# Performance work log

Hardware: AMD Instinct MI355X
Metric: run time of the kernel (lower is better)

The kernel has to match this reference:

```python
import jax, jax.numpy as jnp
import numpy as np

LEAKY_SLOPE = 0.2  # LeakyReLU(0.2) attention activation from the torch module
HEADS = 4
RATES = (10, 25)


def _prod(v):
    r = 1
    for x in v:
        r *= x
    return r


def gat_conv(x_self, x_neigh, W, a_s, a_n):
    """Single GAT aggregation layer (aggregate_method='concat').
    x_self:  [..., F_in]
    x_neigh: [..., E, F_in] (leading dims reshape-compatible with x_self)
    W: [F_in, H*D], a_s/a_n: [H, D]
    Returns [..., H*D].
    """
    H = HEADS
    D = W.shape[1] // H
    lead = x_self.shape[:-1]
    E = x_neigh.shape[-2]
    z_s = (x_self @ W).reshape(lead + (H, D))                  # [..., H, D]
    z_n = (x_neigh @ W).reshape(lead + (E, H, D))              # [..., E, H, D]
    e_s = jnp.einsum('...hd,hd->...h', z_s, a_s)               # [..., H]
    e_n = jnp.einsum('...ehd,hd->...eh', z_n, a_n)             # [..., E, H]
    logits = jax.nn.leaky_relu(e_s[..., None, :] + e_n, LEAKY_SLOPE)
    alpha = jax.nn.softmax(logits, axis=-2)                    # softmax over neighbors E
    out = jnp.einsum('...eh,...ehd->...hd', alpha, z_n)        # attention-weighted sum
    return out.reshape(lead + (H * D,))


def setup_inputs() -> dict:
    key = jax.random.key(0)
    ks = jax.random.split(key, 10)
    B, F, HID, OUT = 1024, 128, 512, 256
    s = 0.05
    return {
        'h0': jax.random.normal(ks[0], (B, F), jnp.float32),
        'h1': jax.random.normal(ks[1], (B, RATES[0], F), jnp.float32),
        'h2': jax.random.normal(ks[2], (B, RATES[0] * RATES[1], F), jnp.float32),
        'W0': jax.random.normal(ks[3], (F, HID), jnp.float32) * s,
        'a0_s': jax.random.normal(ks[4], (HEADS, HID // HEADS), jnp.float32) * s,
        'a0_n': jax.random.normal(ks[5], (HEADS, HID // HEADS), jnp.float32) * s,
        'W1': jax.random.normal(ks[6], (HID, HID), jnp.float32) * s,
        'a1_s': jax.random.normal(ks[7], (HEADS, HID // HEADS), jnp.float32) * s,
        'a1_n': jax.random.normal(ks[8], (HEADS, HID // HEADS), jnp.float32) * s,
        'W_fc': jax.random.normal(ks[9], (HID, OUT), jnp.float32) * s,
    }


def reference(h0, h1, h2, W0, a0_s, a0_n, W1, a1_s, a1_n, W_fc):
    B = h0.shape[0]
    hs = [h0, h1, h2]
    layers = [(W0, a0_s, a0_n), (W1, a1_s, a1_n)]
    depth = len(RATES)
    # hierarchical sweep: layer i is applied to levels 0..depth-i-1
    for i, (W, a_s, a_n) in enumerate(layers):
        for j in range(depth - i):
            x_self = hs[j]
            x_neigh = hs[j + 1].reshape(B, _prod(RATES[:j]), RATES[j], -1)
            hs[j] = gat_conv(x_self, x_neigh, W, a_s, a_n)
    return hs[0] @ W_fc  # final Linear (no bias, no activation)
```

## Files before the change

kernel.cpp:

```cpp
#include <hip/hip_runtime.h>

__global__ void __launch_bounds__(256) prep1(
    const float* __restrict__ W0, const float* __restrict__ a0s,
    const float* __restrict__ a0n,
    const float* __restrict__ W1, const float* __restrict__ a1s,
    const float* __restrict__ a1n, const float* __restrict__ Wfc,
    float* __restrict__ wa0s, float* __restrict__ wa0n,
    float* __restrict__ wa1s, float* __restrict__ wa1n,
    float* __restrict__ T) {
  int idx = blockIdx.x * 256 + threadIdx.x;
  if (idx < 5120) {
    const float* W; const float* a; float* dst; int i; int FIN;
    if (idx < 512)       { W = W0; a = a0s; dst = wa0s; i = idx;        FIN = 128; }
    else if (idx < 1024) { W = W0; a = a0n; dst = wa0n; i = idx - 512;  FIN = 128; }
    else if (idx < 3072) { W = W1; a = a1s; dst = wa1s; i = idx - 1024; FIN = 512; }
    else                 { W = W1; a = a1n; dst = wa1n; i = idx - 3072; FIN = 512; }
    int f = i >> 2, h = i & 3;
    const float* wrow = W + (size_t)f * 512 + h * 128;
    const float* arow = a + h * 128;
    float v = 0.f;
#pragma unroll 8
    for (int d = 0; d < 128; ++d) v = fmaf(wrow[d], arow[d], v);
    dst[h * FIN + f] = v;
    return;
  }
  int j = idx - 5120;
  if (j >= 4 * 512 * 256) return;
  int h = j >> 17;
  int k = (j >> 8) & 511;
  int o = j & 255;
  const float* w1row = W1 + (size_t)k * 512 + h * 128;
  const float* fcol = Wfc + (size_t)h * 128 * 256 + o;
  float v = 0.f;
#pragma unroll 8
  for (int m = 0; m < 128; ++m) v = fmaf(w1row[m], fcol[(size_t)m * 256], v);
  T[j] = v;
}

__global__ void __launch_bounds__(256) prep2(
    const float* __restrict__ W0, const float* __restrict__ wa1s,
    const float* __restrict__ wa1n, const float* __restrict__ T,
    float* __restrict__ va1s, float* __restrict__ va1n,
    float* __restrict__ Wfinal) {
  int idx = blockIdx.x * 256 + threadIdx.x;
  if (idx < 4096) {
    const float* wa = (idx < 2048) ? wa1s : wa1n;
    float* dst = (idx < 2048) ? va1s : va1n;
    int i = idx & 2047;
    int h = i >> 9, h0 = (i >> 7) & 3, f = i & 127;
    const float* w0row = W0 + (size_t)f * 512 + h0 * 128;
    const float* warow = wa + h * 512 + h0 * 128;
    float v = 0.f;
#pragma unroll 8
    for (int n = 0; n < 128; ++n) v = fmaf(w0row[n], warow[n], v);
    dst[i] = v;
    return;
  }
  int j = idx - 4096;
  if (j >= 4 * 512 * 256) return;
  int h = j >> 17;
  int kk = (j >> 8) & 511;
  int o = j & 255;
  int h0 = kk >> 7, f = kk & 127;
  const float* w0row = W0 + (size_t)f * 512 + h0 * 128;
  const float* tcol = T + (size_t)h * 512 * 256 + (size_t)(h0 * 128) * 256 + o;
  float v = 0.f;
#pragma unroll 8
  for (int n = 0; n < 128; ++n) v = fmaf(w0row[n], tcol[(size_t)n * 256], v);
  Wfinal[j] = v;
}

template <int FIN, int MR, int TPR>
__device__ __forceinline__ void gat_body(
    const float* __restrict__ xself, const float* __restrict__ xneigh,
    const float* __restrict__ waS, const float* __restrict__ waN,
    float* __restrict__ out, int E) {
  constexpr int RPP = 256 / TPR;
  constexpr int PSTR = TPR + 1;
  constexpr int G = TPR / 4;
  __shared__ float tile[MR * FIN];
  __shared__ float partial[MR * PSTR];
  __shared__ float logitS[MR * 4];
  __shared__ float alpha[(MR - 1) * 4];
  const int t = threadIdx.x;
  const int el = t / TPR;
  const int f0 = (t % TPR) * 4;
  float4 wn[4], ws[4];
#pragma unroll
  for (int h = 0; h < 4; ++h) {
    wn[h] = *reinterpret_cast<const float4*>(waN + h * FIN + f0);
    ws[h] = *reinterpret_cast<const float4*>(waS + h * FIN + f0);
  }
  const int rows = E + 1;
  for (int p = 0; p * RPP < rows; ++p) {
    int e = p * RPP + el;
    if (e < rows) {
      const float* src = (e < E) ? (xneigh + (size_t)e * FIN + f0) : (xself + f0);
      float4 x = *reinterpret_cast<const float4*>(src);
      *reinterpret_cast<float4*>(tile + e * FIN + f0) = x;
      float ph[4];
#pragma unroll
      for (int h = 0; h < 4; ++h) {
        float4 w = (e < E) ? wn[h] : ws[h];
        ph[h] = x.x * w.x + x.y * w.y + x.z * w.z + x.w * w.w;
      }
#pragma unroll
      for (int h = 0; h < 4; ++h) {
        ph[h] += __shfl_xor(ph[h], 1);
        ph[h] += __shfl_xor(ph[h], 2);
      }
      if ((t & 3) == 0) {
        int g = (t % TPR) >> 2;
        *reinterpret_cast<float4*>(partial + e * PSTR + g * 4) =
            make_float4(ph[0], ph[1], ph[2], ph[3]);
      }
    }
  }
  __syncthreads();
  if (t < rows * 4) {
    int e = t >> 2, h = t & 3;
    float v = 0.f;
#pragma unroll
    for (int g = 0; g < G; ++g) v += partial[e * PSTR + g * 4 + h];
    logitS[t] = v;
  }
  __syncthreads();
  if (t < 4) {
    const float es = logitS[E * 4 + t];
    float m = -1e30f;
    for (int e = 0; e < E; ++e) {
      float x = es + logitS[e * 4 + t];
      x = (x > 0.f) ? x : 0.2f * x;
      m = fmaxf(m, x);
    }
    float s = 0.f;
    for (int e = 0; e < E; ++e) {
      float x = es + logitS[e * 4 + t];
      x = (x > 0.f) ? x : 0.2f * x;
      float p = __expf(x - m);
      alpha[e * 4 + t] = p;
      s += p;
    }
    float inv = 1.f / s;
    for (int e = 0; e < E; ++e) alpha[e * 4 + t] *= inv;
  }
  __syncthreads();
  constexpr int C = FIN / 4;
  for (int o = t; o < 4 * C; o += 256) {
    int h = o / C, f = (o % C) * 4;
    float4 acc = make_float4(0.f, 0.f, 0.f, 0.f);
#pragma unroll 5
    for (int e = 0; e < E; ++e) {
      float a = alpha[e * 4 + h];
      float4 x = *reinterpret_cast<const float4*>(tile + e * FIN + f);
      acc.x = fmaf(a, x.x, acc.x);
      acc.y = fmaf(a, x.y, acc.y);
      acc.z = fmaf(a, x.z, acc.z);
      acc.w = fmaf(a, x.w, acc.w);
    }
    *reinterpret_cast<float4*>(out + h * FIN + f) = acc;
  }
}

__global__ void __launch_bounds__(256) gat_layer0(
    const float* __restrict__ h0, const float* __restrict__ h1,
    const float* __restrict__ h2, const float* __restrict__ waS,
    const float* __restrict__ waN, float* __restrict__ xagg) {
  const int b = blockIdx.x;
  const float* xself;
  const float* xneigh;
  int E;
  if (b < 1024) {
    E = 10;
    xself = h0 + (size_t)b * 128;
    xneigh = h1 + (size_t)b * 10 * 128;
  } else {
    int g = b - 1024;
    E = 25;
    xself = h1 + (size_t)g * 128;
    xneigh = h2 + (size_t)g * 25 * 128;
  }
  gat_body<128, 26, 32>(xself, xneigh, waS, waN, xagg + (size_t)b * 512, E);
}

__global__ void __launch_bounds__(256) gat_layer1(
    const float* __restrict__ xagg0, const float* __restrict__ xagg1,
    const float* __restrict__ vaS, const float* __restrict__ vaN,
    float* __restrict__ aggx) {
  const int b = blockIdx.x;
  gat_body<512, 11, 128>(xagg0 + (size_t)b * 512, xagg1 + (size_t)b * 10 * 512,
                         vaS, vaN, aggx + (size_t)b * 2048, 10);
}

__global__ void __launch_bounds__(256) gemm_ksplit(
    const float* __restrict__ A, int lda,
    const float* __restrict__ B, int ldb,
    float* __restrict__ Cpart, int ldc, int Kchunk) {
  __shared__ float As[16][68];
  __shared__ float Bs[16][132];
  const int m0 = blockIdx.x * 64;
  const int hb = blockIdx.y;
  const int ks = blockIdx.z;
  const int col0 = hb * 128;
  const float* Ab = A + (size_t)m0 * lda + (size_t)ks * Kchunk;
  const float* Bb = B + (size_t)ks * Kchunk * ldb + col0;
  float* Cb = Cpart + (size_t)ks * 1024 * 256;
  const int t = threadIdx.x;
  const int tn = t & 31, tm = t >> 5;
  const int lam = t >> 2, lak = (t & 3) * 4;
  const int lbk = t >> 4, lbn = (t & 15) * 8;
  float acc[8][4];
#pragma unroll
  for (int i = 0; i < 8; ++i)
#pragma unroll
    for (int j = 0; j < 4; ++j) acc[i][j] = 0.f;
  for (int k0 = 0; k0 < Kchunk; k0 += 16) {
    float4 av = *reinterpret_cast<const float4*>(Ab + (size_t)lam * lda + k0 + lak);
    As[lak + 0][lam] = av.x;
    As[lak + 1][lam] = av.y;
    As[lak + 2][lam] = av.z;
    As[lak + 3][lam] = av.w;
    const float* bp = Bb + (size_t)(k0 + lbk) * ldb + lbn;
    float4 b0 = *reinterpret_cast<const float4*>(bp);
    float4 b1 = *reinterpret_cast<const float4*>(bp + 4);
    float* bd = &Bs[lbk][lbn];
    bd[0] = b0.x; bd[1] = b0.y; bd[2] = b0.z; bd[3] = b0.w;
    bd[4] = b1.x; bd[5] = b1.y; bd[6] = b1.z; bd[7] = b1.w;
    __syncthreads();
#pragma unroll
    for (int kk = 0; kk < 16; ++kk) {
      float4 a0 = *reinterpret_cast<const float4*>(&As[kk][tm * 8]);
      float4 a1 = *reinterpret_cast<const float4*>(&As[kk][tm * 8 + 4]);
      float4 bv = *reinterpret_cast<const float4*>(&Bs[kk][tn * 4]);
      float a[8] = {a0.x, a0.y, a0.z, a0.w, a1.x, a1.y, a1.z, a1.w};
      float b[4] = {bv.x, bv.y, bv.z, bv.w};
#pragma unroll
      for (int i = 0; i < 8; ++i)
#pragma unroll
        for (int j = 0; j < 4; ++j) acc[i][j] = fmaf(a[i], b[j], acc[i][j]);
    }
    __syncthreads();
  }
#pragma unroll
  for (int i = 0; i < 8; ++i) {
    const int m = m0 + tm * 8 + i;
    float* cp = Cb + (size_t)m * ldc + col0 + tn * 4;
    *reinterpret_cast<float4*>(cp) =
        make_float4(acc[i][0], acc[i][1], acc[i][2], acc[i][3]);
  }
}

__global__ void __launch_bounds__(256) reduce8(
    const float* __restrict__ Cpart, float* __restrict__ out) {
  int i = blockIdx.x * 256 + threadIdx.x;
  const float4* p = reinterpret_cast<const float4*>(Cpart) + i;
  float4 s = p[0];
#pragma unroll
  for (int ks = 1; ks < 8; ++ks) {
    float4 v = p[(size_t)ks * 65536];
    s.x += v.x; s.y += v.y; s.z += v.z; s.w += v.w;
  }
  reinterpret_cast<float4*>(out)[i] = s;
}

extern "C" void kernel_launch(void* const* d_in, const int* in_sizes, int n_in,
                              void* d_out, int out_size, void* d_ws, size_t ws_size,
                              hipStream_t stream) {
  const float* h0  = (const float*)d_in[0];
  const float* h1  = (const float*)d_in[1];
  const float* h2  = (const float*)d_in[2];
  const float* W0  = (const float*)d_in[3];
  const float* a0s = (const float*)d_in[4];
  const float* a0n = (const float*)d_in[5];
  const float* W1  = (const float*)d_in[6];
  const float* a1s = (const float*)d_in[7];
  const float* a1n = (const float*)d_in[8];
  const float* Wfc = (const float*)d_in[9];
  float* out = (float*)d_out;

  float* ws = (float*)d_ws;
  float* wa0s   = ws;
  float* wa0n   = wa0s + 512;
  float* wa1s   = wa0n + 512;
  float* wa1n   = wa1s + 2048;
  float* va1s   = wa1n + 2048;
  float* va1n   = va1s + 2048;
  float* T      = va1n + 2048;
  float* Wfinal = T + 524288;
  float* xaggA  = Wfinal + 524288;
  float* aggx   = xaggA + 11264 * 512;
  float* Cpart  = aggx + 2097152;

  prep1<<<2068, 256, 0, stream>>>(W0, a0s, a0n, W1, a1s, a1n, Wfc,
                                  wa0s, wa0n, wa1s, wa1n, T);
  prep2<<<2064, 256, 0, stream>>>(W0, wa1s, wa1n, T, va1s, va1n, Wfinal);
  gat_layer0<<<11264, 256, 0, stream>>>(h0, h1, h2, wa0s, wa0n, xaggA);
  gat_layer1<<<1024, 256, 0, stream>>>(xaggA, xaggA + (size_t)1024 * 512,
                                       va1s, va1n, aggx);
  gemm_ksplit<<<dim3(16, 2, 8), 256, 0, stream>>>(aggx, 2048, Wfinal, 256,
                                                  Cpart, 256, 256);
  reduce8<<<256, 256, 0, stream>>>(Cpart, out);
}
```

Baseline: 297.8 us.

## Tile weight-folding prep as GEMMs and fuse into GAT layer-0 launch

```diff
diff --git a/kernel.cpp b/kernel.cpp
--- a/kernel.cpp
+++ b/kernel.cpp
@@ -1,87 +1,71 @@
 #include <hip/hip_runtime.h>
 
-__global__ void __launch_bounds__(256) prep1(
-    const float* __restrict__ W0, const float* __restrict__ a0s,
-    const float* __restrict__ a0n,
-    const float* __restrict__ W1, const float* __restrict__ a1s,
-    const float* __restrict__ a1n, const float* __restrict__ Wfc,
-    float* __restrict__ wa0s, float* __restrict__ wa0n,
-    float* __restrict__ wa1s, float* __restrict__ wa1n,
-    float* __restrict__ T) {
-  int idx = blockIdx.x * 256 + threadIdx.x;
-  if (idx < 5120) {
-    const float* W; const float* a; float* dst; int i; int FIN;
-    if (idx < 512)       { W = W0; a = a0s; dst = wa0s; i = idx;        FIN = 128; }
-    else if (idx < 1024) { W = W0; a = a0n; dst = wa0n; i = idx - 512;  FIN = 128; }
-    else if (idx < 3072) { W = W1; a = a1s; dst = wa1s; i = idx - 1024; FIN = 512; }
-    else                 { W = W1; a = a1n; dst = wa1n; i = idx - 3072; FIN = 512; }
-    int f = i >> 2, h = i & 3;
-    const float* wrow = W + (size_t)f * 512 + h * 128;
-    const float* arow = a + h * 128;
-    float v = 0.f;
-#pragma unroll 8
-    for (int d = 0; d < 128; ++d) v = fmaf(wrow[d], arow[d], v);
-    dst[h * FIN + f] = v;
-    return;
-  }
-  int j = idx - 5120;
-  if (j >= 4 * 512 * 256) return;
-  int h = j >> 17;
-  int k = (j >> 8) & 511;
-  int o = j & 255;
-  const float* w1row = W1 + (size_t)k * 512 + h * 128;
-  const float* fcol = Wfc + (size_t)h * 128 * 256 + o;
-  float v = 0.f;
-#pragma unroll 8
-  for (int m = 0; m < 128; ++m) v = fmaf(w1row[m], fcol[(size_t)m * 256], v);
-  T[j] = v;
-}
-
-__global__ void __launch_bounds__(256) prep2(
-    const float* __restrict__ W0, const float* __restrict__ wa1s,
-    const float* __restrict__ wa1n, const float* __restrict__ T,
-    float* __restrict__ va1s, float* __restrict__ va1n,
-    float* __restrict__ Wfinal) {
-  int idx = blockIdx.x * 256 + threadIdx.x;
-  if (idx < 4096) {
-    const float* wa = (idx < 2048) ? wa1s : wa1n;
-    float* dst = (idx < 2048) ? va1s : va1n;
-    int i = idx & 2047;
-    int h = i >> 9, h0 = (i >> 7) & 3, f = i & 127;
-    const float* w0row = W0 + (size_t)f * 512 + h0 * 128;
-    const float* warow = wa + h * 512 + h0 * 128;
-    float v = 0.f;
-#pragma unroll 8
-    for (int n = 0; n < 128; ++n) v = fmaf(w0row[n], warow[n], v);
-    dst[i] = v;
-    return;
-  }
-  int j = idx - 4096;
-  if (j >= 4 * 512 * 256) return;
-  int h = j >> 17;
-  int kk = (j >> 8) & 511;
-  int o = j & 255;
-  int h0 = kk >> 7, f = kk & 127;
-  const float* w0row = W0 + (size_t)f * 512 + h0 * 128;
-  const float* tcol = T + (size_t)h * 512 * 256 + (size_t)(h0 * 128) * 256 + o;
-  float v = 0.f;
-#pragma unroll 8
-  for (int n = 0; n < 128; ++n) v = fmaf(w0row[n], tcol[(size_t)n * 256], v);
-  Wfinal[j] = v;
-}
-
-template <int FIN, int MR, int TPR>
+__device__ __forceinline__ void gemm_body(
+    float* __restrict__ smem,
+    const float* __restrict__ A, int lda,
+    const float* __restrict__ B, int ldb,
+    float* __restrict__ C, int ldc, int K,
+    int m0, int col0) {
+  float* As = smem;
+  float* Bs = smem + 16 * 68;
+  const int t = threadIdx.x;
+  const int tn = t & 31, tm = t >> 5;
+  const int lam = t >> 2, lak = (t & 3) * 4;
+  const int lbk = t >> 4, lbn = (t & 15) * 8;
+  float acc[8][4];
+#pragma unroll
+  for (int i = 0; i < 8; ++i)
+#pragma unroll
+    for (int j = 0; j < 4; ++j) acc[i][j] = 0.f;
+  for (int k0 = 0; k0 < K; k0 += 16) {
+    float4 av = *reinterpret_cast<const float4*>(A + (size_t)(m0 + lam) * lda + k0 + lak);
+    As[(lak + 0) * 68 + lam] = av.x;
+    As[(lak + 1) * 68 + lam] = av.y;
+    As[(lak + 2) * 68 + lam] = av.z;
+    As[(lak + 3) * 68 + lam] = av.w;
+    const float* bp = B + (size_t)(k0 + lbk) * ldb + col0 + lbn;
+    float4 b0 = *reinterpret_cast<const float4*>(bp);
+    float4 b1 = *reinterpret_cast<const float4*>(bp + 4);
+    float* bd = &Bs[lbk * 132 + lbn];
+    bd[0] = b0.x; bd[1] = b0.y; bd[2] = b0.z; bd[3] = b0.w;
+    bd[4] = b1.x; bd[5] = b1.y; bd[6] = b1.z; bd[7] = b1.w;
+    __syncthreads();
+#pragma unroll
+    for (int kk = 0; kk < 16; ++kk) {
+      float4 a0 = *reinterpret_cast<const float4*>(&As[kk * 68 + tm * 8]);
+      float4 a1 = *reinterpret_cast<const float4*>(&As[kk * 68 + tm * 8 + 4]);
+      float4 bv = *reinterpret_cast<const float4*>(&Bs[kk * 132 + tn * 4]);
+      float a[8] = {a0.x, a0.y, a0.z, a0.w, a1.x, a1.y, a1.z, a1.w};
+      float b[4] = {bv.x, bv.y, bv.z, bv.w};
+#pragma unroll
+      for (int i = 0; i < 8; ++i)
+#pragma unroll
+        for (int j = 0; j < 4; ++j) acc[i][j] = fmaf(a[i], b[j], acc[i][j]);
+    }
+    __syncthreads();
+  }
+#pragma unroll
+  for (int i = 0; i < 8; ++i) {
+    float* cp = C + (size_t)(m0 + tm * 8 + i) * ldc + col0 + tn * 4;
+    *reinterpret_cast<float4*>(cp) =
+        make_float4(acc[i][0], acc[i][1], acc[i][2], acc[i][3]);
+  }
+}
+
+template <int FIN, int TPR, int E>
 __device__ __forceinline__ void gat_body(
+    float* __restrict__ smem,
     const float* __restrict__ xself, const float* __restrict__ xneigh,
     const float* __restrict__ waS, const float* __restrict__ waN,
-    float* __restrict__ out, int E) {
+    float* __restrict__ out) {
+  constexpr int MR = E + 1;
   constexpr int RPP = 256 / TPR;
   constexpr int PSTR = TPR + 1;
   constexpr int G = TPR / 4;
-  __shared__ float tile[MR * FIN];
-  __shared__ float partial[MR * PSTR];
-  __shared__ float logitS[MR * 4];
-  __shared__ float alpha[(MR - 1) * 4];
+  float* tile = smem;
+  float* partial = tile + MR * FIN;
+  float* logitS = partial + MR * PSTR;
+  float* alpha = logitS + MR * 4;
   const int t = threadIdx.x;
   const int el = t / TPR;
   const int f0 = (t % TPR) * 4;
@@ -91,10 +75,10 @@
     wn[h] = *reinterpret_cast<const float4*>(waN + h * FIN + f0);
     ws[h] = *reinterpret_cast<const float4*>(waS + h * FIN + f0);
   }
-  const int rows = E + 1;
-  for (int p = 0; p * RPP < rows; ++p) {
+#pragma unroll
+  for (int p = 0; p * RPP < MR; ++p) {
     int e = p * RPP + el;
-    if (e < rows) {
+    if (e < MR) {
       const float* src = (e < E) ? (xneigh + (size_t)e * FIN + f0) : (xself + f0);
       float4 x = *reinterpret_cast<const float4*>(src);
       *reinterpret_cast<float4*>(tile + e * FIN + f0) = x;
@@ -117,7 +101,7 @@
     }
   }
   __syncthreads();
-  if (t < rows * 4) {
+  if (t < MR * 4) {
     int e = t >> 2, h = t & 3;
     float v = 0.f;
 #pragma unroll
@@ -128,12 +112,14 @@
   if (t < 4) {
     const float es = logitS[E * 4 + t];
     float m = -1e30f;
+#pragma unroll
     for (int e = 0; e < E; ++e) {
       float x = es + logitS[e * 4 + t];
       x = (x > 0.f) ? x : 0.2f * x;
       m = fmaxf(m, x);
     }
     float s = 0.f;
+#pragma unroll
     for (int e = 0; e < E; ++e) {
       float x = es + logitS[e * 4 + t];
       x = (x > 0.f) ? x : 0.2f * x;
@@ -142,6 +128,7 @@
       s += p;
     }
     float inv = 1.f / s;
+#pragma unroll
     for (int e = 0; e < E; ++e) alpha[e * 4 + t] *= inv;
   }
   __syncthreads();
@@ -149,7 +136,7 @@
   for (int o = t; o < 4 * C; o += 256) {
     int h = o / C, f = (o % C) * 4;
     float4 acc = make_float4(0.f, 0.f, 0.f, 0.f);
-#pragma unroll 5
+#pragma unroll
     for (int e = 0; e < E; ++e) {
       float a = alpha[e * 4 + h];
       float4 x = *reinterpret_cast<const float4*>(tile + e * FIN + f);
@@ -162,92 +149,101 @@
   }
 }
 
-__global__ void __launch_bounds__(256) gat_layer0(
+__global__ void __launch_bounds__(256) prepA(
+    const float* __restrict__ W0, const float* __restrict__ a0s,
+    const float* __restrict__ a0n,
+    const float* __restrict__ W1, const float* __restrict__ a1s,
+    const float* __restrict__ a1n, const float* __restrict__ Wfc,
+    float* __restrict__ wa0s, float* __restrict__ wa0n,
+    float* __restrict__ wa1s, float* __restrict__ wa1n,
+    float* __restrict__ T) {
+  __shared__ float smem[3200];
+  const int b = blockIdx.x;
+  if (b < 64) {
+    int h = b >> 4, mb = (b >> 1) & 7, nb = b & 1;
+    gemm_body(smem, W1 + h * 128, 512, Wfc + (size_t)h * 32768, 256,
+              T + (size_t)h * 131072, 256, 128, mb * 64, nb * 128);
+    return;
+  }
+  int idx = (b - 64) * 256 + threadIdx.x;
+  if (idx >= 5120) return;
+  const float* W; const float* a; float* dst; int i; int FIN;
+  if (idx < 512)       { W = W0; a = a0s; dst = wa0s; i = idx;        FIN = 128; }
+  else if (idx < 1024) { W = W0; a = a0n; dst = wa0n; i = idx - 512;  FIN = 128; }
+  else if (idx < 3072) { W = W1; a = a1s; dst = wa1s; i = idx - 1024; FIN = 512; }
+  else                 { W = W1; a = a1n; dst = wa1n; i = idx - 3072; FIN = 512; }
+  int f = i >> 2, h = i & 3;
+  const float* wrow = W + (size_t)f * 512 + h * 128;
+  const float* arow = a + h * 128;
+  float v = 0.f;
+#pragma unroll 8
+  for (int d = 0; d < 128; ++d) v = fmaf(wrow[d], arow[d], v);
+  dst[h * FIN + f] = v;
+}
+
+__global__ void __launch_bounds__(256) fusedB(
     const float* __restrict__ h0, const float* __restrict__ h1,
-    const float* __restrict__ h2, const float* __restrict__ waS,
-    const float* __restrict__ waN, float* __restrict__ xagg) {
+    const float* __restrict__ h2, const float* __restrict__ wa0s,
+    const float* __restrict__ wa0n, float* __restrict__ xagg,
+    const float* __restrict__ W0, const float* __restrict__ wa1s,
+    const float* __restrict__ wa1n, const float* __restrict__ T,
+    float* __restrict__ va1s, float* __restrict__ va1n,
+    float* __restrict__ Wfinal) {
+  __shared__ float smem[4390];
   const int b = blockIdx.x;
-  const float* xself;
-  const float* xneigh;
-  int E;
   if (b < 1024) {
-    E = 10;
-    xself = h0 + (size_t)b * 128;
-    xneigh = h1 + (size_t)b * 10 * 128;
-  } else {
+    gat_body<128, 32, 10>(smem, h0 + (size_t)b * 128, h1 + (size_t)b * 1280,
+                          wa0s, wa0n, xagg + (size_t)b * 512);
+    return;
+  }
+  if (b < 11264) {
     int g = b - 1024;
-    E = 25;
-    xself = h1 + (size_t)g * 128;
-    xneigh = h2 + (size_t)g * 25 * 128;
-  }
-  gat_body<128, 26, 32>(xself, xneigh, waS, waN, xagg + (size_t)b * 512, E);
+    gat_body<128, 32, 25>(smem, h1 + (size_t)g * 128, h2 + (size_t)g * 3200,
+                          wa0s, wa0n, xagg + (size_t)b * 512);
+    return;
+  }
+  if (b < 11264 + 64) {
+    int g = b - 11264;
+    int pair = g >> 2, mb = (g >> 1) & 1, nb = g & 1;
+    int h = pair >> 2, h0b = pair & 3;
+    gemm_body(smem, W0 + h0b * 128, 512,
+              T + (size_t)h * 131072 + (size_t)h0b * 32768, 256,
+              Wfinal + (size_t)h * 131072 + (size_t)h0b * 32768, 256, 128,
+              mb * 64, nb * 128);
+    return;
+  }
+  int idx = (b - 11328) * 256 + threadIdx.x;
+  if (idx >= 4096) return;
+  const float* wa = (idx < 2048) ? wa1s : wa1n;
+  float* dst = (idx < 2048) ? va1s : va1n;
+  int i = idx & 2047;
+  int h = i >> 9, h0b = (i >> 7) & 3, f = i & 127;
+  const float* w0row = W0 + (size_t)f * 512 + h0b * 128;
+  const float* warow = wa + h * 512 + h0b * 128;
+  float v = 0.f;
+#pragma unroll 8
+  for (int n = 0; n < 128; ++n) v = fmaf(w0row[n], warow[n], v);
+  dst[i] = v;
 }
 
 __global__ void __launch_bounds__(256) gat_layer1(
-    const float* __restrict__ xagg0, const float* __restrict__ xagg1,
-    const float* __restrict__ vaS, const float* __restrict__ vaN,
-    float* __restrict__ aggx) {
+    const float* __restrict__ xagg, const float* __restrict__ vaS,
+    const float* __restrict__ vaN, float* __restrict__ aggx) {
+  __shared__ float smem[7135];
   const int b = blockIdx.x;
-  gat_body<512, 11, 128>(xagg0 + (size_t)b * 512, xagg1 + (size_t)b * 10 * 512,
-                         vaS, vaN, aggx + (size_t)b * 2048, 10);
+  gat_body<512, 128, 10>(smem, xagg + (size_t)b * 512,
+                         xagg + (size_t)(1024 + b * 10) * 512, vaS, vaN,
+                         aggx + (size_t)b * 2048);
 }
 
 __global__ void __launch_bounds__(256) gemm_ksplit(
-    const float* __restrict__ A, int lda,
-    const float* __restrict__ B, int ldb,
-    float* __restrict__ Cpart, int ldc, int Kchunk) {
-  __shared__ float As[16][68];
-  __shared__ float Bs[16][132];
-  const int m0 = blockIdx.x * 64;
-  const int hb = blockIdx.y;
+    const float* __restrict__ A, const float* __restrict__ B,
+    float* __restrict__ Cpart) {
+  __shared__ float smem[3200];
   const int ks = blockIdx.z;
-  const int col0 = hb * 128;
-  const float* Ab = A + (size_t)m0 * lda + (size_t)ks * Kchunk;
-  const float* Bb = B + (size_t)ks * Kchunk * ldb + col0;
-  float* Cb = Cpart + (size_t)ks * 1024 * 256;
-  const int t = threadIdx.x;
-  const int tn = t & 31, tm = t >> 5;
-  const int lam = t >> 2, lak = (t & 3) * 4;
-  const int lbk = t >> 4, lbn = (t & 15) * 8;
-  float acc[8][4];
-#pragma unroll
-  for (int i = 0; i < 8; ++i)
-#pragma unroll
-    for (int j = 0; j < 4; ++j) acc[i][j] = 0.f;
-  for (int k0 = 0; k0 < Kchunk; k0 += 16) {
-    float4 av = *reinterpret_cast<const float4*>(Ab + (size_t)lam * lda + k0 + lak);
-    As[lak + 0][lam] = av.x;
-    As[lak + 1][lam] = av.y;
-    As[lak + 2][lam] = av.z;
-    As[lak + 3][lam] = av.w;
-    const float* bp = Bb + (size_t)(k0 + lbk) * ldb + lbn;
-    float4 b0 = *reinterpret_cast<const float4*>(bp);
-    float4 b1 = *reinterpret_cast<const float4*>(bp + 4);
-    float* bd = &Bs[lbk][lbn];
-    bd[0] = b0.x; bd[1] = b0.y; bd[2] = b0.z; bd[3] = b0.w;
-    bd[4] = b1.x; bd[5] = b1.y; bd[6] = b1.z; bd[7] = b1.w;
-    __syncthreads();
-#pragma unroll
-    for (int kk = 0; kk < 16; ++kk) {
-      float4 a0 = *reinterpret_cast<const float4*>(&As[kk][tm * 8]);
-      float4 a1 = *reinterpret_cast<const float4*>(&As[kk][tm * 8 + 4]);
-      float4 bv = *reinterpret_cast<const float4*>(&Bs[kk][tn * 4]);
-      float a[8] = {a0.x, a0.y, a0.z, a0.w, a1.x, a1.y, a1.z, a1.w};
-      float b[4] = {bv.x, bv.y, bv.z, bv.w};
-#pragma unroll
-      for (int i = 0; i < 8; ++i)
-#pragma unroll
-        for (int j = 0; j < 4; ++j) acc[i][j] = fmaf(a[i], b[j], acc[i][j]);
-    }
-    __syncthreads();
-  }
-#pragma unroll
-  for (int i = 0; i < 8; ++i) {
-    const int m = m0 + tm * 8 + i;
-    float* cp = Cb + (size_t)m * ldc + col0 + tn * 4;
-    *reinterpret_cast<float4*>(cp) =
-        make_float4(acc[i][0], acc[i][1], acc[i][2], acc[i][3]);
-  }
+  gemm_body(smem, A + ks * 256, 2048, B + (size_t)ks * 65536, 256,
+            Cpart + (size_t)ks * 262144, 256, 256, blockIdx.x * 64,
+            blockIdx.y * 128);
 }
 
 __global__ void __launch_bounds__(256) reduce8(
@@ -291,13 +287,11 @@
   float* aggx   = xaggA + 11264 * 512;
   float* Cpart  = aggx + 2097152;
 
-  prep1<<<2068, 256, 0, stream>>>(W0, a0s, a0n, W1, a1s, a1n, Wfc,
-                                  wa0s, wa0n, wa1s, wa1n, T);
-  prep2<<<2064, 256, 0, stream>>>(W0, wa1s, wa1n, T, va1s, va1n, Wfinal);
-  gat_layer0<<<11264, 256, 0, stream>>>(h0, h1, h2, wa0s, wa0n, xaggA);
-  gat_layer1<<<1024, 256, 0, stream>>>(xaggA, xaggA + (size_t)1024 * 512,
-                                       va1s, va1n, aggx);
-  gemm_ksplit<<<dim3(16, 2, 8), 256, 0, stream>>>(aggx, 2048, Wfinal, 256,
-                                                  Cpart, 256, 256);
+  prepA<<<84, 256, 0, stream>>>(W0, a0s, a0n, W1, a1s, a1n, Wfc,
+                                wa0s, wa0n, wa1s, wa1n, T);
+  fusedB<<<11344, 256, 0, stream>>>(h0, h1, h2, wa0s, wa0n, xaggA,
+                                    W0, wa1s, wa1n, T, va1s, va1n, Wfinal);
+  gat_layer1<<<1024, 256, 0, stream>>>(xaggA, va1s, va1n, aggx);
+  gemm_ksplit<<<dim3(16, 2, 8), 256, 0, stream>>>(aggx, Wfinal, Cpart);
   reduce8<<<256, 256, 0, stream>>>(Cpart, out);
 }
```

Result: faster. 269.9 us, median of 2 (-9.4%).
